# Optimization experiments

Measured on AMD Instinct MI355X. Metric: run time of the kernel, lower is better.

The kernel has to match this reference:

```python
import jax, jax.numpy as jnp
import numpy as np
import math

N_NEURONS = 2048
MAX_MEMORY = 32
BATCH = 128

def setup_inputs() -> dict:
    key = jax.random.key(0)
    k1, k2, k3 = jax.random.split(key, 3)
    state_trace = jax.random.normal(k1, (BATCH, N_NEURONS, MAX_MEMORY), dtype=jnp.float32)
    fc1_weight = jax.random.normal(k2, (N_NEURONS, MAX_MEMORY, 256), dtype=jnp.float32) * math.sqrt(2.0 / MAX_MEMORY)
    fc1_bias = jnp.zeros((N_NEURONS, 256), dtype=jnp.float32)
    fc2_weight = jax.random.normal(k3, (N_NEURONS, 128, 2), dtype=jnp.float32) * math.sqrt(2.0 / 128)
    fc2_bias = jnp.zeros((N_NEURONS, 2), dtype=jnp.float32)
    T = jnp.ones((1,), dtype=jnp.float32)
    return {"state_trace": state_trace, "fc1_weight": fc1_weight, "fc1_bias": fc1_bias,
            "fc2_weight": fc2_weight, "fc2_bias": fc2_bias, "T": T}

def _glu(x):
    # torch F.glu(dim=-1): first half * sigmoid(second half)
    a, b = jnp.split(x, 2, axis=-1)
    return a * jax.nn.sigmoid(b)

def reference(state_trace, fc1_weight, fc1_bias, fc2_weight, fc2_bias, T):
    # per-neuron batched GEMM 1: (b,n,m) x (n,m,256) -> (b,n,256)
    x_fc1 = jnp.einsum('bnm,nmh->bnh', state_trace, fc1_weight) + fc1_bias
    x_glu1 = _glu(x_fc1)                                   # (b, n, 128)
    # per-neuron batched GEMM 2: (b,n,128) x (n,128,2) -> (b,n,2)
    x_fc2 = jnp.einsum('bnh,nho->bno', x_glu1, fc2_weight) + fc2_bias
    x_glu2 = _glu(x_fc2)                                   # (b, n, 1)
    return jnp.squeeze(x_glu2, -1) / T                     # (b, n)
```

## Files before the change

### kernel.cpp

```cpp
#include <hip/hip_runtime.h>
#include <hip/hip_bf16.h>


#define NN 2048

typedef __attribute__((ext_vector_type(8))) short short8;
typedef __attribute__((ext_vector_type(4))) float floatx4;
typedef __attribute__((ext_vector_type(4))) int int4v;

static __device__ __forceinline__ unsigned int pkbf(float a, float b) {
    __hip_bfloat162 h = __float22bfloat162_rn(make_float2(a, b));
    return *(unsigned int*)&h;
}

static __device__ __forceinline__ float sigmoidf(float x) {
    return 1.0f / (1.0f + __expf(-x));
}

static __device__ __forceinline__ void gload_lds16(const float* g, float* l) {
    __builtin_amdgcn_global_load_lds((const __attribute__((address_space(1))) void*)g,
                                     (__attribute__((address_space(3))) void*)l,
                                     16, 0, 0);
}

__global__ __launch_bounds__(256, 2)
void nlm_kernel(const float* __restrict__ st,
                const float* __restrict__ w1,
                const float* __restrict__ b1,
                const float* __restrict__ w2,
                const float* __restrict__ b2,
                const float* __restrict__ Tp,
                float* __restrict__ out_t)
{
    const int n = blockIdx.x;
    const int t = threadIdx.x;

    __shared__ __align__(16) float  ldsW[32 * 256];
    __shared__ short  ldsB[16 * 64 * 8];
    __shared__ float4 ldsP[128];
    __shared__ float  ldsO[128];

    const int lane = t & 63;
    const int wv   = t >> 6;
    const int m    = lane & 15;
    const int quad = lane >> 4;

    {
        const float* gW = w1 + (size_t)n * 8192;
        #pragma unroll
        for (int i = 0; i < 8; ++i) {
            const int off = wv * 2048 + i * 256;
            gload_lds16(gW + off + lane * 4, &ldsW[off]);
        }
    }

    floatx4 av[2][2];
    #pragma unroll
    for (int bt = 0; bt < 2; ++bt) {
        const int b = wv * 32 + bt * 16 + m;
        const float* sp = st + (size_t)b * (NN * 32) + (size_t)n * 32 + quad * 8;
        av[bt][0] = *(const floatx4*)sp;
        av[bt][1] = *(const floatx4*)(sp + 4);
    }

    const float* b1p = b1 + n * 256;
    const float* w2p = w2 + n * 256;
    float pba = 0.f, pbb = 0.f;
    float2 pw2 = make_float2(0.f, 0.f);
    if (t < 128) {
        pba = b1p[t];
        pbb = b1p[128 + t];
        pw2 = *(const float2*)(w2p + 2 * t);
    }

    const float bb0  = b2[n * 2 + 0];
    const float bb1  = b2[n * 2 + 1];
    const float invT = 1.0f / Tp[0];

    short8 afrag[2];
    #pragma unroll
    for (int bt = 0; bt < 2; ++bt) {
        union { int4v i; short8 s; } u;
        u.i[0] = pkbf(av[bt][0][0], av[bt][0][1]);
        u.i[1] = pkbf(av[bt][0][2], av[bt][0][3]);
        u.i[2] = pkbf(av[bt][1][0], av[bt][1][1]);
        u.i[3] = pkbf(av[bt][1][2], av[bt][1][3]);
        afrag[bt] = u.s;
    }
    if (t < 128)
        ldsP[t] = make_float4(pba, pbb, pw2.x, pw2.y);

    __syncthreads();

    {
        const int base = ((t >> 4) * 512) + ((t & 15) * 8);
        #pragma unroll
        for (int q = 0; q < 4; ++q) {
            float w[8];
            #pragma unroll
            for (int j = 0; j < 8; ++j)
                w[j] = ldsW[(q * 8 + j) * 256 + t];
            union { int4v i; short8 s; } u;
            #pragma unroll
            for (int e = 0; e < 4; ++e)
                u.i[e] = pkbf(w[2 * e], w[2 * e + 1]);
            *(short8*)&ldsB[base + q * 128] = u.s;
        }
    }

    __syncthreads();

    float pacc[2][4][2];
    #pragma unroll
    for (int bt = 0; bt < 2; ++bt)
        #pragma unroll
        for (int r = 0; r < 4; ++r)
            pacc[bt][r][0] = pacc[bt][r][1] = 0.0f;

    #pragma unroll
    for (int p = 0; p < 8; ++p) {
        short8 bfA = *(short8*)&ldsB[(p * 64 + lane) * 8];
        short8 bfB = *(short8*)&ldsB[((p + 8) * 64 + lane) * 8];
        float4 prm = ldsP[p * 16 + m];

        #pragma unroll
        for (int bt = 0; bt < 2; ++bt) {
            floatx4 z = {0.0f, 0.0f, 0.0f, 0.0f};
            floatx4 xa = __builtin_amdgcn_mfma_f32_16x16x32_bf16(afrag[bt], bfA, z, 0, 0, 0);
            floatx4 xb = __builtin_amdgcn_mfma_f32_16x16x32_bf16(afrag[bt], bfB, z, 0, 0, 0);
            #pragma unroll
            for (int r = 0; r < 4; ++r) {
                float a   = xa[r] + prm.x;
                float g   = xb[r] + prm.y;
                float glu = a * sigmoidf(g);
                pacc[bt][r][0] += glu * prm.z;
                pacc[bt][r][1] += glu * prm.w;
            }
        }
    }

    #pragma unroll
    for (int bt = 0; bt < 2; ++bt) {
        #pragma unroll
        for (int r = 0; r < 4; ++r) {
            float s0 = pacc[bt][r][0];
            float s1 = pacc[bt][r][1];
            s0 += __shfl_xor(s0, 1);  s1 += __shfl_xor(s1, 1);
            s0 += __shfl_xor(s0, 2);  s1 += __shfl_xor(s1, 2);
            s0 += __shfl_xor(s0, 4);  s1 += __shfl_xor(s1, 4);
            s0 += __shfl_xor(s0, 8);  s1 += __shfl_xor(s1, 8);
            if (m == 0) {
                const int b = wv * 32 + bt * 16 + quad * 4 + r;
                float x0 = s0 + bb0;
                float x1 = s1 + bb1;
                ldsO[b] = x0 * sigmoidf(x1) * invT;
            }
        }
    }

    __syncthreads();

    if (t < 128)
        out_t[(size_t)n * 128 + t] = ldsO[t];
}

__global__ __launch_bounds__(256)
void transpose_kernel(const float* __restrict__ out_t, float* __restrict__ out)
{
    __shared__ float tile[32][33];
    const int t    = threadIdx.x;
    const int bidx = blockIdx.x;
    const int n0   = (bidx & 63) * 32;
    const int b0   = (bidx >> 6) * 32;

    const int tx = t & 31;
    const int ty = t >> 5;

    #pragma unroll
    for (int i = 0; i < 4; ++i) {
        const int nl = ty + i * 8;
        tile[nl][tx] = out_t[(size_t)(n0 + nl) * 128 + b0 + tx];
    }

    __syncthreads();

    #pragma unroll
    for (int i = 0; i < 4; ++i) {
        const int bl = ty + i * 8;
        out[(size_t)(b0 + bl) * NN + n0 + tx] = tile[tx][bl];
    }
}

extern "C" void kernel_launch(void* const* d_in, const int* in_sizes, int n_in,
                              void* d_out, int out_size, void* d_ws, size_t ws_size,
                              hipStream_t stream) {
    const float* st = (const float*)d_in[0];
    const float* w1 = (const float*)d_in[1];
    const float* b1 = (const float*)d_in[2];
    const float* w2 = (const float*)d_in[3];
    const float* b2 = (const float*)d_in[4];
    const float* T  = (const float*)d_in[5];
    float* out   = (float*)d_out;
    float* out_t = (float*)d_ws;

    nlm_kernel<<<dim3(NN), dim3(256), 0, stream>>>(st, w1, b1, w2, b2, T, out_t);
    transpose_kernel<<<dim3(256), dim3(256), 0, stream>>>(out_t, out);
}
```

Baseline: 144.0 us.

## Process four neurons per block with prefetch of next neuron's weights

Each block now handles NPB=4 neurons in sequence. While one neuron's GEMMs run, it prefetches the next neuron's fc1 weights into LDS, along with its state-trace fragments and bias/fc2 parameters, so global latency overlaps compute. The sigmoid reciprocal also switches to the hardware rcp builtin. The cost is fewer blocks (512 rather than 2048), which on a many-CU GPU may reduce parallelism and latency hiding across blocks.

```diff
diff --git a/kernel.cpp b/kernel.cpp
--- a/kernel.cpp
+++ b/kernel.cpp
@@ -3,6 +3,7 @@
 
 
 #define NN 2048
+#define NPB 4
 
 typedef __attribute__((ext_vector_type(8))) short short8;
 typedef __attribute__((ext_vector_type(4))) float floatx4;
@@ -14,7 +15,7 @@
 }
 
 static __device__ __forceinline__ float sigmoidf(float x) {
-    return 1.0f / (1.0f + __expf(-x));
+    return __builtin_amdgcn_rcpf(1.0f + __expf(-x));
 }
 
 static __device__ __forceinline__ void gload_lds16(const float* g, float* l) {
@@ -32,136 +33,166 @@
                 const float* __restrict__ Tp,
                 float* __restrict__ out_t)
 {
-    const int n = blockIdx.x;
-    const int t = threadIdx.x;
-
-    __shared__ __align__(16) float  ldsW[32 * 256];
-    __shared__ short  ldsB[16 * 64 * 8];
-    __shared__ float4 ldsP[128];
-    __shared__ float  ldsO[128];
+    const int n0 = blockIdx.x * NPB;
+    const int t  = threadIdx.x;
+
+    __shared__ __align__(16) float ldsW[32 * 256];
+    __shared__ __align__(16) short ldsB[16 * 64 * 8];
+    __shared__ float4 ldsP[2][128];
+    __shared__ float  ldsO[NPB][128];
 
     const int lane = t & 63;
     const int wv   = t >> 6;
     const int m    = lane & 15;
     const int quad = lane >> 4;
 
-    {
-        const float* gW = w1 + (size_t)n * 8192;
-        #pragma unroll
-        for (int i = 0; i < 8; ++i) {
-            const int off = wv * 2048 + i * 256;
-            gload_lds16(gW + off + lane * 4, &ldsW[off]);
-        }
-    }
-
-    floatx4 av[2][2];
+    const float* gW0 = w1 + (size_t)n0 * 8192;
+
+    floatx4 av[2][2][2];
+    float  pa_n = 0.f, pb_n = 0.f;
+    float2 pw_n = make_float2(0.f, 0.f);
+
+    #pragma unroll
+    for (int j = 0; j < 8; ++j) {
+        const int off = wv * 2048 + j * 256;
+        gload_lds16(gW0 + off + lane * 4, &ldsW[off]);
+    }
     #pragma unroll
     for (int bt = 0; bt < 2; ++bt) {
         const int b = wv * 32 + bt * 16 + m;
-        const float* sp = st + (size_t)b * (NN * 32) + (size_t)n * 32 + quad * 8;
-        av[bt][0] = *(const floatx4*)sp;
-        av[bt][1] = *(const floatx4*)(sp + 4);
-    }
-
-    const float* b1p = b1 + n * 256;
-    const float* w2p = w2 + n * 256;
-    float pba = 0.f, pbb = 0.f;
-    float2 pw2 = make_float2(0.f, 0.f);
+        const float* sp = st + (size_t)b * (NN * 32) + (size_t)n0 * 32 + quad * 8;
+        av[0][bt][0] = *(const floatx4*)sp;
+        av[0][bt][1] = *(const floatx4*)(sp + 4);
+    }
     if (t < 128) {
-        pba = b1p[t];
-        pbb = b1p[128 + t];
-        pw2 = *(const float2*)(w2p + 2 * t);
-    }
-
-    const float bb0  = b2[n * 2 + 0];
-    const float bb1  = b2[n * 2 + 1];
+        const float* b1p = b1 + n0 * 256;
+        const float* w2p = w2 + n0 * 256;
+        float  pa = b1p[t];
+        float  pb = b1p[128 + t];
+        float2 pw = *(const float2*)(w2p + 2 * t);
+        ldsP[0][t] = make_float4(pa, pb, pw.x, pw.y);
+    }
+
     const float invT = 1.0f / Tp[0];
 
-    short8 afrag[2];
-    #pragma unroll
-    for (int bt = 0; bt < 2; ++bt) {
-        union { int4v i; short8 s; } u;
-        u.i[0] = pkbf(av[bt][0][0], av[bt][0][1]);
-        u.i[1] = pkbf(av[bt][0][2], av[bt][0][3]);
-        u.i[2] = pkbf(av[bt][1][0], av[bt][1][1]);
-        u.i[3] = pkbf(av[bt][1][2], av[bt][1][3]);
-        afrag[bt] = u.s;
-    }
-    if (t < 128)
-        ldsP[t] = make_float4(pba, pbb, pw2.x, pw2.y);
+    #pragma unroll
+    for (int i = 0; i < NPB; ++i) {
+        __syncthreads();
+
+        {
+            const int base = ((t >> 4) * 512) + ((t & 15) * 8);
+            #pragma unroll
+            for (int q = 0; q < 4; ++q) {
+                float w8[8];
+                #pragma unroll
+                for (int j = 0; j < 8; ++j)
+                    w8[j] = ldsW[(q * 8 + j) * 256 + t];
+                union { int4v iv; short8 s; } u;
+                #pragma unroll
+                for (int e = 0; e < 4; ++e)
+                    u.iv[e] = pkbf(w8[2 * e], w8[2 * e + 1]);
+                *(short8*)&ldsB[base + q * 128] = u.s;
+            }
+        }
+
+        __syncthreads();
+
+        if (i + 1 < NPB) {
+            const float* gW = w1 + (size_t)(n0 + i + 1) * 8192;
+            #pragma unroll
+            for (int j = 0; j < 8; ++j) {
+                const int off = wv * 2048 + j * 256;
+                gload_lds16(gW + off + lane * 4, &ldsW[off]);
+            }
+            #pragma unroll
+            for (int bt = 0; bt < 2; ++bt) {
+                const int b = wv * 32 + bt * 16 + m;
+                const float* sp = st + (size_t)b * (NN * 32)
+                                     + (size_t)(n0 + i + 1) * 32 + quad * 8;
+                av[(i + 1) & 1][bt][0] = *(const floatx4*)sp;
+                av[(i + 1) & 1][bt][1] = *(const floatx4*)(sp + 4);
+            }
+            if (t < 128) {
+                const float* b1p = b1 + (n0 + i + 1) * 256;
+                const float* w2p = w2 + (n0 + i + 1) * 256;
+                pa_n = b1p[t];
+                pb_n = b1p[128 + t];
+                pw_n = *(const float2*)(w2p + 2 * t);
+            }
+        }
+
+        short8 afrag[2];
+        #pragma unroll
+        for (int bt = 0; bt < 2; ++bt) {
+            union { int4v iv; short8 s; } u;
+            u.iv[0] = pkbf(av[i & 1][bt][0][0], av[i & 1][bt][0][1]);
+            u.iv[1] = pkbf(av[i & 1][bt][0][2], av[i & 1][bt][0][3]);
+            u.iv[2] = pkbf(av[i & 1][bt][1][0], av[i & 1][bt][1][1]);
+            u.iv[3] = pkbf(av[i & 1][bt][1][2], av[i & 1][bt][1][3]);
+            afrag[bt] = u.s;
+        }
+
+        float pacc[2][4][2];
+        #pragma unroll
+        for (int bt = 0; bt < 2; ++bt)
+            #pragma unroll
+            for (int r = 0; r < 4; ++r)
+                pacc[bt][r][0] = pacc[bt][r][1] = 0.0f;
+
+        #pragma unroll
+        for (int p = 0; p < 8; ++p) {
+            short8 bfA = *(short8*)&ldsB[(p * 64 + lane) * 8];
+            short8 bfB = *(short8*)&ldsB[((p + 8) * 64 + lane) * 8];
+            float4 prm = ldsP[i & 1][p * 16 + m];
+
+            #pragma unroll
+            for (int bt = 0; bt < 2; ++bt) {
+                floatx4 z = {0.0f, 0.0f, 0.0f, 0.0f};
+                floatx4 xa = __builtin_amdgcn_mfma_f32_16x16x32_bf16(afrag[bt], bfA, z, 0, 0, 0);
+                floatx4 xb = __builtin_amdgcn_mfma_f32_16x16x32_bf16(afrag[bt], bfB, z, 0, 0, 0);
+                #pragma unroll
+                for (int r = 0; r < 4; ++r) {
+                    float a   = xa[r] + prm.x;
+                    float g   = xb[r] + prm.y;
+                    float glu = a * sigmoidf(g);
+                    pacc[bt][r][0] += glu * prm.z;
+                    pacc[bt][r][1] += glu * prm.w;
+                }
+            }
+        }
+
+        const float bb0 = b2[(n0 + i) * 2 + 0];
+        const float bb1 = b2[(n0 + i) * 2 + 1];
+
+        #pragma unroll
+        for (int bt = 0; bt < 2; ++bt) {
+            #pragma unroll
+            for (int r = 0; r < 4; ++r) {
+                float s0 = pacc[bt][r][0];
+                float s1 = pacc[bt][r][1];
+                s0 += __shfl_xor(s0, 1);  s1 += __shfl_xor(s1, 1);
+                s0 += __shfl_xor(s0, 2);  s1 += __shfl_xor(s1, 2);
+                s0 += __shfl_xor(s0, 4);  s1 += __shfl_xor(s1, 4);
+                s0 += __shfl_xor(s0, 8);  s1 += __shfl_xor(s1, 8);
+                if (m == 0) {
+                    const int b = wv * 32 + bt * 16 + quad * 4 + r;
+                    float x0 = s0 + bb0;
+                    float x1 = s1 + bb1;
+                    ldsO[i][b] = x0 * sigmoidf(x1) * invT;
+                }
+            }
+        }
+
+        if (i + 1 < NPB && t < 128)
+            ldsP[(i + 1) & 1][t] = make_float4(pa_n, pb_n, pw_n.x, pw_n.y);
+    }
 
     __syncthreads();
 
     {
-        const int base = ((t >> 4) * 512) + ((t & 15) * 8);
-        #pragma unroll
-        for (int q = 0; q < 4; ++q) {
-            float w[8];
-            #pragma unroll
-            for (int j = 0; j < 8; ++j)
-                w[j] = ldsW[(q * 8 + j) * 256 + t];
-            union { int4v i; short8 s; } u;
-            #pragma unroll
-            for (int e = 0; e < 4; ++e)
-                u.i[e] = pkbf(w[2 * e], w[2 * e + 1]);
-            *(short8*)&ldsB[base + q * 128] = u.s;
-        }
-    }
-
-    __syncthreads();
-
-    float pacc[2][4][2];
-    #pragma unroll
-    for (int bt = 0; bt < 2; ++bt)
-        #pragma unroll
-        for (int r = 0; r < 4; ++r)
-            pacc[bt][r][0] = pacc[bt][r][1] = 0.0f;
-
-    #pragma unroll
-    for (int p = 0; p < 8; ++p) {
-        short8 bfA = *(short8*)&ldsB[(p * 64 + lane) * 8];
-        short8 bfB = *(short8*)&ldsB[((p + 8) * 64 + lane) * 8];
-        float4 prm = ldsP[p * 16 + m];
-
-        #pragma unroll
-        for (int bt = 0; bt < 2; ++bt) {
-            floatx4 z = {0.0f, 0.0f, 0.0f, 0.0f};
-            floatx4 xa = __builtin_amdgcn_mfma_f32_16x16x32_bf16(afrag[bt], bfA, z, 0, 0, 0);
-            floatx4 xb = __builtin_amdgcn_mfma_f32_16x16x32_bf16(afrag[bt], bfB, z, 0, 0, 0);
-            #pragma unroll
-            for (int r = 0; r < 4; ++r) {
-                float a   = xa[r] + prm.x;
-                float g   = xb[r] + prm.y;
-                float glu = a * sigmoidf(g);
-                pacc[bt][r][0] += glu * prm.z;
-                pacc[bt][r][1] += glu * prm.w;
-            }
-        }
-    }
-
-    #pragma unroll
-    for (int bt = 0; bt < 2; ++bt) {
-        #pragma unroll
-        for (int r = 0; r < 4; ++r) {
-            float s0 = pacc[bt][r][0];
-            float s1 = pacc[bt][r][1];
-            s0 += __shfl_xor(s0, 1);  s1 += __shfl_xor(s1, 1);
-            s0 += __shfl_xor(s0, 2);  s1 += __shfl_xor(s1, 2);
-            s0 += __shfl_xor(s0, 4);  s1 += __shfl_xor(s1, 4);
-            s0 += __shfl_xor(s0, 8);  s1 += __shfl_xor(s1, 8);
-            if (m == 0) {
-                const int b = wv * 32 + bt * 16 + quad * 4 + r;
-                float x0 = s0 + bb0;
-                float x1 = s1 + bb1;
-                ldsO[b] = x0 * sigmoidf(x1) * invT;
-            }
-        }
-    }
-
-    __syncthreads();
-
-    if (t < 128)
-        out_t[(size_t)n * 128 + t] = ldsO[t];
+        float2* dst = (float2*)(out_t + (size_t)n0 * 128);
+        dst[t] = ((const float2*)ldsO)[t];
+    }
 }
 
 __global__ __launch_bounds__(256)
@@ -203,6 +234,6 @@
     float* out   = (float*)d_out;
     float* out_t = (float*)d_ws;
 
-    nlm_kernel<<<dim3(NN), dim3(256), 0, stream>>>(st, w1, b1, w2, b2, T, out_t);
+    nlm_kernel<<<dim3(NN / NPB), dim3(256), 0, stream>>>(st, w1, b1, w2, b2, T, out_t);
     transpose_kernel<<<dim3(256), dim3(256), 0, stream>>>(out_t, out);
 }
```

Measured after the change: 135.8 us. 1.06x faster.
